# Optimization experiments

Hardware: AMD Instinct MI355X
Metric: run time of the kernel (lower is better)

## Reference

```python
import jax, jax.numpy as jnp
import numpy as np

FILTER_SIZE = 15
BLUR_SIGMA_INIT = 5.0
DIFF_SIGMA_INIT = 1.0


def setup_inputs() -> dict:
    key = jax.random.key(0)
    x = jax.random.normal(key, (2, 3, 224, 224), dtype=jnp.float32)
    blur_sigma = jnp.float32(BLUR_SIGMA_INIT)
    diff_sigma = jnp.float32(DIFF_SIGMA_INIT)
    return {"x": x, "blur_sigma": blur_sigma, "diff_sigma": diff_sigma,
            "filter_size": FILTER_SIZE}


def _squared_distances(k, dtype):
    # distances[i, j] = (i - mid)^2 + (j - mid)^2, flattened row-major (matches unfold)
    mid = k // 2
    r = np.arange(k) - mid
    d = (r[:, None] ** 2 + r[None, :] ** 2).reshape(-1)
    return jnp.asarray(d, dtype=dtype)


def reference(x, blur_sigma, diff_sigma, filter_size):
    k = filter_size
    pad = k // 2
    B, C, H, W = x.shape
    # F.pad(x + 100, ...) - 100 == constant pad with -100
    padded = jnp.pad(x, ((0, 0), (0, 0), (pad, pad), (pad, pad)),
                     constant_values=-100.0)
    # [B, C*k*k, H, W], channel-major ordering (C, then kernel row, then kernel col)
    patches = jax.lax.conv_general_dilated_patches(
        padded, (k, k), (1, 1), 'VALID')
    patches = patches.reshape(B, C, k * k, H, W)
    dist = _squared_distances(k, x.dtype)  # [k*k]
    diffs = (patches - x[:, :, None]) ** 2 / (diff_sigma ** 2)
    blurs = dist[None, None, :, None, None] / (blur_sigma ** 2)
    # exp(-(diffs+blurs)) normalized over window axis == softmax of the negated logits
    probs = jax.nn.softmax(-(diffs + blurs), axis=2)
    return jnp.sum(patches * probs, axis=2)
```

## Files before the change

### kernel.cpp

```cpp
#include <hip/hip_runtime.h>

#define HH 224
#define WW 224
#define K 15
#define PAD 7
#define BX 32
#define BY 8
#define TW (BX + K - 1)
#define TH (BY + K - 1)
#define TSTRIDE 48

__global__ __launch_bounds__(BX * BY)
void bilateral_denoise_kernel(const float* __restrict__ x,
                              const float* __restrict__ blur_sigma_p,
                              const float* __restrict__ diff_sigma_p,
                              float* __restrict__ out)
{
    __shared__ float tile[TH * TSTRIDE];

    const int tx = threadIdx.x;
    const int ty = threadIdx.y;
    const int tid = ty * BX + tx;
    const int w0 = blockIdx.x * BX;
    const int h0 = blockIdx.y * BY;
    const int plane = blockIdx.z;

    const float* __restrict__ xp = x + (size_t)plane * HH * WW;

    for (int idx = tid; idx < TH * TW; idx += BX * BY) {
        const int r = idx / TW;
        const int c = idx - r * TW;
        const int gh = h0 - PAD + r;
        const int gw = w0 - PAD + c;
        float v = -100.0f;
        if (gh >= 0 && gh < HH && gw >= 0 && gw < WW) v = xp[gh * WW + gw];
        tile[r * TSTRIDE + c] = v;
    }
    __syncthreads();

    const float bs = blur_sigma_p[0];
    const float ds = diff_sigma_p[0];
    const float LOG2E = 1.44269504088896340736f;
    const float na  = -LOG2E / (ds * ds);
    const float nk2 = -LOG2E / (bs * bs);

    const float cv = tile[(ty + PAD) * TSTRIDE + tx + PAD];
    const float bb = -2.0f * na * cv;
    const float cc = na * cv * cv;

    float colw[K];
    float colv[K];
#pragma unroll
    for (int j = 0; j < K; ++j) { colw[j] = 0.0f; colv[j] = 0.0f; }

#pragma unroll
    for (int i = 0; i < K; ++i) {
        const float ci = __builtin_fmaf((float)((i - PAD) * (i - PAD)), nk2, cc);
        const float* __restrict__ row = &tile[(ty + i) * TSTRIDE + tx];
#pragma unroll
        for (int j = 0; j < K; ++j) {
            const float v = row[j];
            const float inner = __builtin_fmaf(v, na, bb);
            const float t = __builtin_fmaf(v, inner, ci);
            const float e = __builtin_amdgcn_exp2f(t);
            colw[j] += e;
            colv[j] = __builtin_fmaf(e, v, colv[j]);
        }
    }

    float wsum = 0.0f;
    float vsum = 0.0f;
#pragma unroll
    for (int j = 0; j < K; ++j) {
        const float wj = __builtin_amdgcn_exp2f((float)((j - PAD) * (j - PAD)) * nk2);
        wsum = __builtin_fmaf(wj, colw[j], wsum);
        vsum = __builtin_fmaf(wj, colv[j], vsum);
    }

    out[(size_t)plane * HH * WW + (size_t)(h0 + ty) * WW + (w0 + tx)] = vsum / wsum;
}

extern "C" void kernel_launch(void* const* d_in, const int* in_sizes, int n_in,
                              void* d_out, int out_size, void* d_ws, size_t ws_size,
                              hipStream_t stream) {
    const float* x  = (const float*)d_in[0];
    const float* bs = (const float*)d_in[1];
    const float* ds = (const float*)d_in[2];
    float* out = (float*)d_out;

    const int planes = in_sizes[0] / (HH * WW);
    dim3 grid(WW / BX, HH / BY, planes);
    dim3 block(BX, BY, 1);
    hipLaunchKernelGGL(bilateral_denoise_kernel, grid, block, 0, stream,
                       x, bs, ds, out);
}
```

Before: 20.35 us.

## Split filter window rows across two thread halves with shared-memory reduction

Each block now computes 4 output rows instead of 8. The two halves of its threads process the first 8 and last 7 window rows respectively, and their partial weight and value sums are combined through shared memory. This doubles the grid size to improve CU occupancy and load balance. In exchange it adds an extra barrier and reduction, uneven work between the halves, and more redundant halo loading per output.

```diff
diff --git a/kernel.cpp b/kernel.cpp
--- a/kernel.cpp
+++ b/kernel.cpp
@@ -5,36 +5,40 @@
 #define K 15
 #define PAD 7
 #define BX 32
-#define BY 8
+#define BYO 4
 #define TW (BX + K - 1)
-#define TH (BY + K - 1)
+#define TH2 (BYO + K - 1)
 #define TSTRIDE 48
 
-__global__ __launch_bounds__(BX * BY)
+__global__ __launch_bounds__(BX * 8)
 void bilateral_denoise_kernel(const float* __restrict__ x,
                               const float* __restrict__ blur_sigma_p,
                               const float* __restrict__ diff_sigma_p,
                               float* __restrict__ out)
 {
-    __shared__ float tile[TH * TSTRIDE];
+    __shared__ float tile[TH2 * TSTRIDE];
+    __shared__ float pw[256];
+    __shared__ float pv[256];
 
-    const int tx = threadIdx.x;
-    const int ty = threadIdx.y;
-    const int tid = ty * BX + tx;
+    const int tx   = threadIdx.x;
+    const int ty   = threadIdx.y;
+    const int tid  = ty * BX + tx;
+    const int tyo  = ty & 3;
+    const int half = ty >> 2;
     const int w0 = blockIdx.x * BX;
-    const int h0 = blockIdx.y * BY;
+    const int h0 = blockIdx.y * BYO;
     const int plane = blockIdx.z;
 
     const float* __restrict__ xp = x + (size_t)plane * HH * WW;
 
-    for (int idx = tid; idx < TH * TW; idx += BX * BY) {
-        const int r = idx / TW;
-        const int c = idx - r * TW;
-        const int gh = h0 - PAD + r;
-        const int gw = w0 - PAD + c;
-        float v = -100.0f;
-        if (gh >= 0 && gh < HH && gw >= 0 && gw < WW) v = xp[gh * WW + gw];
-        tile[r * TSTRIDE + c] = v;
+    for (int rr = ty; rr < TH2; rr += 8) {
+        const int gh = h0 - PAD + rr;
+        for (int cc = tx; cc < TW; cc += BX) {
+            const int gw = w0 - PAD + cc;
+            float v = -100.0f;
+            if (gh >= 0 && gh < HH && gw >= 0 && gw < WW) v = xp[gh * WW + gw];
+            tile[rr * TSTRIDE + cc] = v;
+        }
     }
     __syncthreads();
 
@@ -44,27 +48,45 @@
     const float na  = -LOG2E / (ds * ds);
     const float nk2 = -LOG2E / (bs * bs);
 
-    const float cv = tile[(ty + PAD) * TSTRIDE + tx + PAD];
-    const float bb = -2.0f * na * cv;
-    const float cc = na * cv * cv;
+    const float cv = tile[(tyo + PAD) * TSTRIDE + tx + PAD];
+    const float bb  = -2.0f * na * cv;
+    const float cc2 = na * cv * cv;
 
     float colw[K];
     float colv[K];
 #pragma unroll
     for (int j = 0; j < K; ++j) { colw[j] = 0.0f; colv[j] = 0.0f; }
 
+    if (half == 0) {
 #pragma unroll
-    for (int i = 0; i < K; ++i) {
-        const float ci = __builtin_fmaf((float)((i - PAD) * (i - PAD)), nk2, cc);
-        const float* __restrict__ row = &tile[(ty + i) * TSTRIDE + tx];
+        for (int i = 0; i < 8; ++i) {
+            const float ci = __builtin_fmaf((float)((i - PAD) * (i - PAD)), nk2, cc2);
+            const float* __restrict__ row = &tile[(tyo + i) * TSTRIDE + tx];
 #pragma unroll
-        for (int j = 0; j < K; ++j) {
-            const float v = row[j];
-            const float inner = __builtin_fmaf(v, na, bb);
-            const float t = __builtin_fmaf(v, inner, ci);
-            const float e = __builtin_amdgcn_exp2f(t);
-            colw[j] += e;
-            colv[j] = __builtin_fmaf(e, v, colv[j]);
+            for (int j = 0; j < K; ++j) {
+                const float v = row[j];
+                const float inner = __builtin_fmaf(v, na, bb);
+                const float t = __builtin_fmaf(v, inner, ci);
+                const float e = __builtin_amdgcn_exp2f(t);
+                colw[j] += e;
+                colv[j] = __builtin_fmaf(e, v, colv[j]);
+            }
+        }
+    } else {
+#pragma unroll
+        for (int ii = 0; ii < 7; ++ii) {
+            const int i = 8 + ii;
+            const float ci = __builtin_fmaf((float)((i - PAD) * (i - PAD)), nk2, cc2);
+            const float* __restrict__ row = &tile[(tyo + i) * TSTRIDE + tx];
+#pragma unroll
+            for (int j = 0; j < K; ++j) {
+                const float v = row[j];
+                const float inner = __builtin_fmaf(v, na, bb);
+                const float t = __builtin_fmaf(v, inner, ci);
+                const float e = __builtin_amdgcn_exp2f(t);
+                colw[j] += e;
+                colv[j] = __builtin_fmaf(e, v, colv[j]);
+            }
         }
     }
 
@@ -77,7 +99,15 @@
         vsum = __builtin_fmaf(wj, colv[j], vsum);
     }
 
-    out[(size_t)plane * HH * WW + (size_t)(h0 + ty) * WW + (w0 + tx)] = vsum / wsum;
+    pw[tid] = wsum;
+    pv[tid] = vsum;
+    __syncthreads();
+
+    if (ty < BYO) {
+        const float w = pw[tid] + pw[tid + 128];
+        const float v = pv[tid] + pv[tid + 128];
+        out[(size_t)plane * HH * WW + (size_t)(h0 + ty) * WW + (w0 + tx)] = v / w;
+    }
 }
 
 extern "C" void kernel_launch(void* const* d_in, const int* in_sizes, int n_in,
@@ -89,8 +119,8 @@
     float* out = (float*)d_out;
 
     const int planes = in_sizes[0] / (HH * WW);
-    dim3 grid(WW / BX, HH / BY, planes);
-    dim3 block(BX, BY, 1);
+    dim3 grid(WW / BX, HH / BYO, planes);
+    dim3 block(BX, 8, 1);
     hipLaunchKernelGGL(bilateral_denoise_kernel, grid, block, 0, stream,
                        x, bs, ds, out);
 }
```

Result: slower. 21.22 us (+4.3%).

## Pre-pad input into workspace and read neighborhoods directly from global memory

Applied to the files above, without the earlier changes.

Adds a separate kernel that writes a -100-padded copy of the input into the workspace buffer. The bilateral kernel then drops its shared-memory tile, the bounds checks and the __syncthreads, and reads its 15x15 window straight from the padded global buffer through the cache. This adds a second launch and an extra pass over memory, and it relies on L1/L2 to serve the 225 loads per thread that LDS used to serve. It also hardcodes six planes.

```diff
diff --git a/kernel.cpp b/kernel.cpp
--- a/kernel.cpp
+++ b/kernel.cpp
@@ -4,39 +4,44 @@
 #define WW 224
 #define K 15
 #define PAD 7
+#define PH (HH + 2 * PAD)
+#define PSTRIDE 240
+#define NPLANES 6
 #define BX 32
 #define BY 8
-#define TW (BX + K - 1)
-#define TH (BY + K - 1)
-#define TSTRIDE 48
+
+__global__ __launch_bounds__(256)
+void pad_kernel(const float* __restrict__ x, float* __restrict__ xpad)
+{
+    const int idx = blockIdx.x * 256 + threadIdx.x;
+    const int total = NPLANES * PH * PSTRIDE;
+    if (idx >= total) return;
+    const int p   = idx / (PH * PSTRIDE);
+    const int rem = idx - p * (PH * PSTRIDE);
+    const int r   = rem / PSTRIDE;
+    const int c   = rem - r * PSTRIDE;
+    const int gh = r - PAD;
+    const int gw = c - PAD;
+    float v = -100.0f;
+    if (gh >= 0 && gh < HH && gw >= 0 && gw < WW)
+        v = x[(size_t)p * HH * WW + gh * WW + gw];
+    xpad[idx] = v;
+}
 
 __global__ __launch_bounds__(BX * BY)
-void bilateral_denoise_kernel(const float* __restrict__ x,
+void bilateral_denoise_kernel(const float* __restrict__ xpad,
                               const float* __restrict__ blur_sigma_p,
                               const float* __restrict__ diff_sigma_p,
                               float* __restrict__ out)
 {
-    __shared__ float tile[TH * TSTRIDE];
-
     const int tx = threadIdx.x;
     const int ty = threadIdx.y;
-    const int tid = ty * BX + tx;
     const int w0 = blockIdx.x * BX;
-    const int h0 = blockIdx.y * BY;
+    const int h  = blockIdx.y * BY + ty;
     const int plane = blockIdx.z;
 
-    const float* __restrict__ xp = x + (size_t)plane * HH * WW;
-
-    for (int idx = tid; idx < TH * TW; idx += BX * BY) {
-        const int r = idx / TW;
-        const int c = idx - r * TW;
-        const int gh = h0 - PAD + r;
-        const int gw = w0 - PAD + c;
-        float v = -100.0f;
-        if (gh >= 0 && gh < HH && gw >= 0 && gw < WW) v = xp[gh * WW + gw];
-        tile[r * TSTRIDE + c] = v;
-    }
-    __syncthreads();
+    const float* __restrict__ base =
+        xpad + (size_t)plane * PH * PSTRIDE + (size_t)h * PSTRIDE + (w0 + tx);
 
     const float bs = blur_sigma_p[0];
     const float ds = diff_sigma_p[0];
@@ -44,9 +49,9 @@
     const float na  = -LOG2E / (ds * ds);
     const float nk2 = -LOG2E / (bs * bs);
 
-    const float cv = tile[(ty + PAD) * TSTRIDE + tx + PAD];
-    const float bb = -2.0f * na * cv;
-    const float cc = na * cv * cv;
+    const float cv = base[PAD * PSTRIDE + PAD];
+    const float bb  = -2.0f * na * cv;
+    const float cc2 = na * cv * cv;
 
     float colw[K];
     float colv[K];
@@ -55,8 +60,8 @@
 
 #pragma unroll
     for (int i = 0; i < K; ++i) {
-        const float ci = __builtin_fmaf((float)((i - PAD) * (i - PAD)), nk2, cc);
-        const float* __restrict__ row = &tile[(ty + i) * TSTRIDE + tx];
+        const float ci = __builtin_fmaf((float)((i - PAD) * (i - PAD)), nk2, cc2);
+        const float* __restrict__ row = base + i * PSTRIDE;
 #pragma unroll
         for (int j = 0; j < K; ++j) {
             const float v = row[j];
@@ -77,7 +82,7 @@
         vsum = __builtin_fmaf(wj, colv[j], vsum);
     }
 
-    out[(size_t)plane * HH * WW + (size_t)(h0 + ty) * WW + (w0 + tx)] = vsum / wsum;
+    out[(size_t)plane * HH * WW + (size_t)h * WW + (w0 + tx)] = vsum / wsum;
 }
 
 extern "C" void kernel_launch(void* const* d_in, const int* in_sizes, int n_in,
@@ -86,11 +91,15 @@
     const float* x  = (const float*)d_in[0];
     const float* bs = (const float*)d_in[1];
     const float* ds = (const float*)d_in[2];
-    float* out = (float*)d_out;
+    float* out  = (float*)d_out;
+    float* xpad = (float*)d_ws;
 
-    const int planes = in_sizes[0] / (HH * WW);
-    dim3 grid(WW / BX, HH / BY, planes);
+    const int total = NPLANES * PH * PSTRIDE;
+    hipLaunchKernelGGL(pad_kernel, dim3((total + 255) / 256), dim3(256), 0, stream,
+                       x, xpad);
+
+    dim3 grid(WW / BX, HH / BY, NPLANES);
     dim3 block(BX, BY, 1);
     hipLaunchKernelGGL(bilateral_denoise_kernel, grid, block, 0, stream,
-                       x, bs, ds, out);
+                       xpad, bs, ds, out);
 }
```

Measured after the change: 25.70 us. 26.3% more time.
